# Kernel tuning notes

Measured on AMD Instinct MI355X. Metric: run time of the kernel, lower is better.

## Reference

```python
import jax, jax.numpy as jnp
import numpy as np

PATCH_SIZE = 3
CHANNELS = 1
SIGMA_RAW = 0.5
SIGMA_EFF = SIGMA_RAW * PATCH_SIZE ** 2  # sigma * patch_size**2 as in __init__


def setup_inputs() -> dict:
    key = jax.random.key(0)
    kx, ky = jax.random.split(key)
    N, C, H, W = 64, CHANNELS, 64, 64
    x = jax.random.normal(kx, (N, C, H, W), dtype=jnp.float32)
    y = jax.random.normal(ky, (N, C, H, W), dtype=jnp.float32)
    return {"x": x, "y": y}


def _pairwise_patch_distance(A, B):
    # A: (N_A, C, H, W), B: (N_B, C, H, W)
    N_A, C, H, W = A.shape
    N_B = B.shape[0]
    # broadcast pairwise squared pixel diffs: (N_A, N_B, C, H, W)
    pixel_diff = (A[:, None] - B[None]) ** 2
    kern = jnp.ones((1, C, PATCH_SIZE, PATCH_SIZE), dtype=A.dtype)  # OIHW
    d = jax.lax.conv_general_dilated(
        pixel_diff.reshape(N_A * N_B, C, H, W), kern,
        window_strides=(1, 1), padding='VALID',
        dimension_numbers=('NCHW', 'OIHW', 'NCHW'))
    H_new, W_new = d.shape[-2], d.shape[-1]
    return d.reshape(N_A, N_B, H_new, W_new)


def _gaussian_kernel(D):
    return jnp.exp(-D / (2.0 * SIGMA_EFF ** 2))


def _off_mean(K):
    # K: (N, N, h, w); mean over all off-diagonal (i != j) entries
    N, _, h, w = K.shape
    mask = ~jnp.eye(N, dtype=bool)
    total = jnp.sum(jnp.where(mask[:, :, None, None], K, jnp.zeros((), K.dtype)))
    count = (N * (N - 1)) * h * w
    return total / count


def reference(x, y):
    K_xx = _gaussian_kernel(_pairwise_patch_distance(x, x))
    K_xy = _gaussian_kernel(_pairwise_patch_distance(x, y))
    K_yy = _gaussian_kernel(_pairwise_patch_distance(y, y))
    return _off_mean(K_xx) - 2.0 * jnp.mean(K_xy) + _off_mean(K_yy)
```

## Files before the change

kernel.cpp:

```cpp
#include <hip/hip_runtime.h>


typedef __attribute__((ext_vector_type(8))) short short8v;
typedef __attribute__((ext_vector_type(4))) float f32x4;

#define NPOS 3844
#define WSTR 26
#define NBLK 992

#if __has_builtin(__builtin_amdgcn_exp2f)
#define EXP2F(v) __builtin_amdgcn_exp2f(v)
#else
#define EXP2F(v) __expf((v) * 0.69314718055994530942f)
#endif

template<int CTRL>
__device__ __forceinline__ float dpp0_f(float v) {
    int r = __builtin_amdgcn_update_dpp(0, __float_as_int(v), CTRL, 0xf, 0xf, true);
    return __int_as_float(r);
}
template<int CTRL, int RM>
__device__ __forceinline__ float dppm_f(float v) {
    int r = __builtin_amdgcn_update_dpp(0, __float_as_int(v), CTRL, RM, 0xf, true);
    return __int_as_float(r);
}
__device__ __forceinline__ float wave_reduce_f(float v) {
    v += dpp0_f<0x111>(v);
    v += dpp0_f<0x112>(v);
    v += dpp0_f<0x114>(v);
    v += dpp0_f<0x118>(v);
    v += dppm_f<0x142, 0xa>(v);
    v += dppm_f<0x143, 0xc>(v);
    return v;
}
__device__ __forceinline__ unsigned int bf16rne(float f) {
    unsigned int u = __float_as_uint(f);
    return (u + 0x7fffu + ((u >> 16) & 1u)) >> 16;
}

__global__ __launch_bounds__(256, 4) void mmd_fused_kernel(
    const float* __restrict__ x, const float* __restrict__ y,
    float* __restrict__ part)
{
    const int t = threadIdx.x, wid = t >> 6, lane = t & 63;
    const int p  = blockIdx.x >> 4;
    const int qg = blockIdx.x & 15;
    const int q  = qg * 4 + wid;

    __shared__ unsigned short win[128 * WSTR];
    __shared__ unsigned short rec[4 * 128 * 8];
    __shared__ unsigned short rec8[4 * 128];
    __shared__ float pren[4 * 128];
    __shared__ float wred[3][4];

    const float NS   = -1.0f / (40.5f * 0.69314718055994530942f);
    const float M2NS = -2.0f * NS;

    {
        const int cg1 = (qg < 15) ? qg + 1 : 15;
        #pragma unroll
        for (int k = 0; k < 3; ++k) {
            int it = t + k * 256;
            int n = it / 6, rem = it % 6;
            int u = rem >> 1, cg = rem & 1;
            const float* img = (n < 64) ? (x + n * 4096) : (y + (n - 64) * 4096);
            float4 v = *reinterpret_cast<const float4*>(
                img + (p + u) * 64 + ((cg ? cg1 : qg) << 2));
            unsigned int d0 = bf16rne(v.x) | (bf16rne(v.y) << 16);
            unsigned int d1 = bf16rne(v.z) | (bf16rne(v.w) << 16);
            unsigned int* w32 = reinterpret_cast<unsigned int*>(
                &win[n * WSTR + u * 8 + cg * 4]);
            w32[0] = d0; w32[1] = d1;
        }
    }
    __syncthreads();

    #pragma unroll
    for (int k = 0; k < 2; ++k) {
        int rid = t + k * 256;
        int ql = rid >> 7, n = rid & 127;
        const unsigned short* wp = &win[n * WSTR + ql];
        unsigned short b[9];
        #pragma unroll
        for (int u = 0; u < 3; ++u) {
            b[u * 3 + 0] = wp[u * 8 + 0];
            b[u * 3 + 1] = wp[u * 8 + 1];
            b[u * 3 + 2] = wp[u * 8 + 2];
        }
        float pre = 0.f;
        #pragma unroll
        for (int e = 0; e < 9; ++e) {
            float fv = __uint_as_float((unsigned)b[e] << 16);
            pre = fmaf(fv, fv, pre);
        }
        uint4 pk;
        pk.x = b[0] | ((unsigned)b[1] << 16);
        pk.y = b[2] | ((unsigned)b[3] << 16);
        pk.z = b[4] | ((unsigned)b[5] << 16);
        pk.w = b[6] | ((unsigned)b[7] << 16);
        *reinterpret_cast<uint4*>(&rec[(size_t)rid * 8]) = pk;
        rec8[rid] = b[8];
        pren[rid] = pre * NS;
    }
    __syncthreads();

    const int r = lane & 15, kg = lane >> 4;
    short8v frag[8];
    #pragma unroll
    for (int g = 0; g < 8; ++g) {
        short8v f = {0, 0, 0, 0, 0, 0, 0, 0};
        if (kg == 0)
            f = *reinterpret_cast<const short8v*>(&rec[(size_t)(wid * 128 + g * 16 + r) * 8]);
        else if (kg == 1)
            f[0] = (short)rec8[wid * 128 + g * 16 + r];
        frag[g] = f;
    }
    float pa[8][4], pb[8];
    #pragma unroll
    for (int g = 0; g < 8; ++g) {
        const float* pp = &pren[wid * 128 + g * 16 + kg * 4];
        pa[g][0] = pp[0]; pa[g][1] = pp[1]; pa[g][2] = pp[2]; pa[g][3] = pp[3];
        pb[g] = pren[wid * 128 + g * 16 + r];
    }

    const f32x4 zf = {0.f, 0.f, 0.f, 0.f};
    float ad0 = 0.f, ad1 = 0.f, as0 = 0.f, as1 = 0.f, ac0 = 0.f, ac1 = 0.f;

    #pragma unroll
    for (int g = 0; g < 8; ++g) {
        f32x4 c4 = __builtin_amdgcn_mfma_f32_16x16x32_bf16(frag[g], frag[g], zf, 0, 0, 0);
        float e = 0.f;
        #pragma unroll
        for (int m = 0; m < 4; ++m)
            e += EXP2F(fmaf(c4[m], M2NS, pa[g][m] + pb[g]));
        if (g & 1) ad1 += e; else ad0 += e;
    }

    #pragma unroll
    for (int ti = 1; ti < 8; ++ti)
        #pragma unroll
        for (int tj = 0; tj < ti; ++tj) {
            f32x4 c4 = __builtin_amdgcn_mfma_f32_16x16x32_bf16(frag[ti], frag[tj], zf, 0, 0, 0);
            float e = 0.f;
            #pragma unroll
            for (int m = 0; m < 4; ++m)
                e += EXP2F(fmaf(c4[m], M2NS, pa[ti][m] + pb[tj]));
            if (ti >= 4 && tj < 4) { if (tj & 1) ac1 += e; else ac0 += e; }
            else                   { if (tj & 1) as1 += e; else as0 += e; }
        }

    float acc_diag  = wave_reduce_f(ad0 + ad1);
    float acc_same  = wave_reduce_f(as0 + as1);
    float acc_cross = wave_reduce_f(ac0 + ac1);
    if (lane == 63) {
        const bool valid = (q < 62);
        wred[0][wid] = valid ? acc_diag  : 0.f;
        wred[1][wid] = valid ? acc_same  : 0.f;
        wred[2][wid] = valid ? acc_cross : 0.f;
    }
    __syncthreads();
    if (t == 0) {
        #pragma unroll
        for (int c = 0; c < 3; ++c)
            part[c * NBLK + blockIdx.x] =
                (wred[c][0] + wred[c][1]) + (wred[c][2] + wred[c][3]);
    }
}

__global__ __launch_bounds__(256) void mmd_final_kernel(
    const float* __restrict__ part, float* __restrict__ out)
{
    const int t = threadIdx.x;
    double sd = 0.0, ss = 0.0, sc = 0.0;
    #pragma unroll
    for (int k = 0; k < 4; ++k) {
        int e = t + k * 256;
        if (e < NBLK) {
            sd += (double)part[e];
            ss += (double)part[NBLK + e];
            sc += (double)part[2 * NBLK + e];
        }
    }
    #pragma unroll
    for (int off = 32; off > 0; off >>= 1) {
        sd += __shfl_xor(sd, off);
        ss += __shfl_xor(ss, off);
        sc += __shfl_xor(sc, off);
    }
    __shared__ double w[3][4];
    const int lane = t & 63, wd = t >> 6;
    if (lane == 0) { w[0][wd] = sd; w[1][wd] = ss; w[2][wd] = sc; }
    __syncthreads();
    if (t == 0) {
        double Sd = w[0][0] + w[0][1] + w[0][2] + w[0][3];
        double Ss = w[1][0] + w[1][1] + w[1][2] + w[1][3];
        double Sc = w[2][0] + w[2][1] + w[2][2] + w[2][3];
        double S_off = (Sd - 128.0 * (double)NPOS) + 2.0 * Ss;
        const double cnt_off = 64.0 * 63.0 * 62.0 * 62.0;
        const double cnt_all = 64.0 * 64.0 * 62.0 * 62.0;
        out[0] = (float)(S_off / cnt_off - 2.0 * Sc / cnt_all);
    }
}

extern "C" void kernel_launch(void* const* d_in, const int* in_sizes, int n_in,
                              void* d_out, int out_size, void* d_ws, size_t ws_size,
                              hipStream_t stream) {
    const float* x = (const float*)d_in[0];
    const float* y = (const float*)d_in[1];
    float* out  = (float*)d_out;
    float* part = (float*)d_ws;

    mmd_fused_kernel<<<62 * 16, 256, 0, stream>>>(x, y, part);
    mmd_final_kernel<<<1, 256, 0, stream>>>(part, out);
}
```

Measured before the change: 18.01 us.

## Switch to f16 MFMA and fold final reduction into main kernel via atomics

Replaces the bf16 16x16x32 MFMA with the f16 16x16x16 MFMA, padding each 9-element patch to 16 halves so each lane loads a 4-half fragment without branching. It also removes the second reduction kernel: each block atomically adds its three partial sums into global doubles, and the last block (found via an atomic counter) computes the output. This drops one kernel launch but adds a memset, atomics and a fence, and f16 changes the precision and range of the inputs.

```diff
diff --git a/kernel.cpp b/kernel.cpp
--- a/kernel.cpp
+++ b/kernel.cpp
@@ -1,7 +1,8 @@
 #include <hip/hip_runtime.h>
+#include <hip/hip_fp16.h>
 
 
-typedef __attribute__((ext_vector_type(8))) short short8v;
+typedef __attribute__((ext_vector_type(4))) _Float16 half4v;
 typedef __attribute__((ext_vector_type(4))) float f32x4;
 
 #define NPOS 3844
@@ -33,14 +34,19 @@
     v += dppm_f<0x143, 0xc>(v);
     return v;
 }
-__device__ __forceinline__ unsigned int bf16rne(float f) {
-    unsigned int u = __float_as_uint(f);
-    return (u + 0x7fffu + ((u >> 16) & 1u)) >> 16;
+__device__ __forceinline__ unsigned short f16bits(float f) {
+    __half h = __float2half(f);
+    return *reinterpret_cast<unsigned short*>(&h);
+}
+__device__ __forceinline__ float f16tof(unsigned short u) {
+    __half h = *reinterpret_cast<__half*>(&u);
+    return __half2float(h);
 }
 
 __global__ __launch_bounds__(256, 4) void mmd_fused_kernel(
     const float* __restrict__ x, const float* __restrict__ y,
-    float* __restrict__ part)
+    double* __restrict__ gacc, unsigned int* __restrict__ gcnt,
+    float* __restrict__ out)
 {
     const int t = threadIdx.x, wid = t >> 6, lane = t & 63;
     const int p  = blockIdx.x >> 4;
@@ -48,8 +54,7 @@
     const int q  = qg * 4 + wid;
 
     __shared__ unsigned short win[128 * WSTR];
-    __shared__ unsigned short rec[4 * 128 * 8];
-    __shared__ unsigned short rec8[4 * 128];
+    __shared__ unsigned short rec[4 * 128 * 16];
     __shared__ float pren[4 * 128];
     __shared__ float wred[3][4];
 
@@ -66,8 +71,8 @@
             const float* img = (n < 64) ? (x + n * 4096) : (y + (n - 64) * 4096);
             float4 v = *reinterpret_cast<const float4*>(
                 img + (p + u) * 64 + ((cg ? cg1 : qg) << 2));
-            unsigned int d0 = bf16rne(v.x) | (bf16rne(v.y) << 16);
-            unsigned int d1 = bf16rne(v.z) | (bf16rne(v.w) << 16);
+            unsigned int d0 = f16bits(v.x) | ((unsigned)f16bits(v.y) << 16);
+            unsigned int d1 = f16bits(v.z) | ((unsigned)f16bits(v.w) << 16);
             unsigned int* w32 = reinterpret_cast<unsigned int*>(
                 &win[n * WSTR + u * 8 + cg * 4]);
             w32[0] = d0; w32[1] = d1;
@@ -90,7 +95,7 @@
         float pre = 0.f;
         #pragma unroll
         for (int e = 0; e < 9; ++e) {
-            float fv = __uint_as_float((unsigned)b[e] << 16);
+            float fv = f16tof(b[e]);
             pre = fmaf(fv, fv, pre);
         }
         uint4 pk;
@@ -98,23 +103,21 @@
         pk.y = b[2] | ((unsigned)b[3] << 16);
         pk.z = b[4] | ((unsigned)b[5] << 16);
         pk.w = b[6] | ((unsigned)b[7] << 16);
-        *reinterpret_cast<uint4*>(&rec[(size_t)rid * 8]) = pk;
-        rec8[rid] = b[8];
+        uint4 pk2;
+        pk2.x = (unsigned)b[8]; pk2.y = 0u; pk2.z = 0u; pk2.w = 0u;
+        uint4* dst = reinterpret_cast<uint4*>(&rec[(size_t)rid * 16]);
+        dst[0] = pk; dst[1] = pk2;
         pren[rid] = pre * NS;
     }
     __syncthreads();
 
     const int r = lane & 15, kg = lane >> 4;
-    short8v frag[8];
+    half4v frag[8];
     #pragma unroll
-    for (int g = 0; g < 8; ++g) {
-        short8v f = {0, 0, 0, 0, 0, 0, 0, 0};
-        if (kg == 0)
-            f = *reinterpret_cast<const short8v*>(&rec[(size_t)(wid * 128 + g * 16 + r) * 8]);
-        else if (kg == 1)
-            f[0] = (short)rec8[wid * 128 + g * 16 + r];
-        frag[g] = f;
-    }
+    for (int g = 0; g < 8; ++g)
+        frag[g] = *reinterpret_cast<const half4v*>(
+            &rec[(size_t)(wid * 128 + g * 16 + r) * 16 + kg * 4]);
+
     float pa[8][4], pb[8];
     #pragma unroll
     for (int g = 0; g < 8; ++g) {
@@ -128,7 +131,7 @@
 
     #pragma unroll
     for (int g = 0; g < 8; ++g) {
-        f32x4 c4 = __builtin_amdgcn_mfma_f32_16x16x32_bf16(frag[g], frag[g], zf, 0, 0, 0);
+        f32x4 c4 = __builtin_amdgcn_mfma_f32_16x16x16f16(frag[g], frag[g], zf, 0, 0, 0);
         float e = 0.f;
         #pragma unroll
         for (int m = 0; m < 4; ++m)
@@ -140,7 +143,7 @@
     for (int ti = 1; ti < 8; ++ti)
         #pragma unroll
         for (int tj = 0; tj < ti; ++tj) {
-            f32x4 c4 = __builtin_amdgcn_mfma_f32_16x16x32_bf16(frag[ti], frag[tj], zf, 0, 0, 0);
+            f32x4 c4 = __builtin_amdgcn_mfma_f32_16x16x16f16(frag[ti], frag[tj], zf, 0, 0, 0);
             float e = 0.f;
             #pragma unroll
             for (int m = 0; m < 4; ++m)
@@ -159,46 +162,25 @@
         wred[2][wid] = valid ? acc_cross : 0.f;
     }
     __syncthreads();
+
     if (t == 0) {
-        #pragma unroll
-        for (int c = 0; c < 3; ++c)
-            part[c * NBLK + blockIdx.x] =
-                (wred[c][0] + wred[c][1]) + (wred[c][2] + wred[c][3]);
-    }
-}
-
-__global__ __launch_bounds__(256) void mmd_final_kernel(
-    const float* __restrict__ part, float* __restrict__ out)
-{
-    const int t = threadIdx.x;
-    double sd = 0.0, ss = 0.0, sc = 0.0;
-    #pragma unroll
-    for (int k = 0; k < 4; ++k) {
-        int e = t + k * 256;
-        if (e < NBLK) {
-            sd += (double)part[e];
-            ss += (double)part[NBLK + e];
-            sc += (double)part[2 * NBLK + e];
+        double sd = (double)((wred[0][0] + wred[0][1]) + (wred[0][2] + wred[0][3]));
+        double ss = (double)((wred[1][0] + wred[1][1]) + (wred[1][2] + wred[1][3]));
+        double sc = (double)((wred[2][0] + wred[2][1]) + (wred[2][2] + wred[2][3]));
+        atomicAdd(&gacc[0], sd);
+        atomicAdd(&gacc[1], ss);
+        atomicAdd(&gacc[2], sc);
+        __threadfence();
+        unsigned int tick = atomicAdd(gcnt, 1u);
+        if (tick == NBLK - 1) {
+            double Sd = atomicAdd(&gacc[0], 0.0);
+            double Ss = atomicAdd(&gacc[1], 0.0);
+            double Sc = atomicAdd(&gacc[2], 0.0);
+            double S_off = (Sd - 128.0 * (double)NPOS) + 2.0 * Ss;
+            const double cnt_off = 64.0 * 63.0 * 62.0 * 62.0;
+            const double cnt_all = 64.0 * 64.0 * 62.0 * 62.0;
+            out[0] = (float)(S_off / cnt_off - 2.0 * Sc / cnt_all);
         }
-    }
-    #pragma unroll
-    for (int off = 32; off > 0; off >>= 1) {
-        sd += __shfl_xor(sd, off);
-        ss += __shfl_xor(ss, off);
-        sc += __shfl_xor(sc, off);
-    }
-    __shared__ double w[3][4];
-    const int lane = t & 63, wd = t >> 6;
-    if (lane == 0) { w[0][wd] = sd; w[1][wd] = ss; w[2][wd] = sc; }
-    __syncthreads();
-    if (t == 0) {
-        double Sd = w[0][0] + w[0][1] + w[0][2] + w[0][3];
-        double Ss = w[1][0] + w[1][1] + w[1][2] + w[1][3];
-        double Sc = w[2][0] + w[2][1] + w[2][2] + w[2][3];
-        double S_off = (Sd - 128.0 * (double)NPOS) + 2.0 * Ss;
-        const double cnt_off = 64.0 * 63.0 * 62.0 * 62.0;
-        const double cnt_all = 64.0 * 64.0 * 62.0 * 62.0;
-        out[0] = (float)(S_off / cnt_off - 2.0 * Sc / cnt_all);
     }
 }
 
@@ -207,9 +189,10 @@
                               hipStream_t stream) {
     const float* x = (const float*)d_in[0];
     const float* y = (const float*)d_in[1];
-    float* out  = (float*)d_out;
-    float* part = (float*)d_ws;
+    float* out = (float*)d_out;
+    double* gacc = (double*)d_ws;
+    unsigned int* gcnt = (unsigned int*)(gacc + 3);
 
-    mmd_fused_kernel<<<62 * 16, 256, 0, stream>>>(x, y, part);
-    mmd_final_kernel<<<1, 256, 0, stream>>>(part, out);
+    (void)hipMemsetAsync(d_ws, 0, 32, stream);
+    mmd_fused_kernel<<<NBLK, 256, 0, stream>>>(x, y, gacc, gcnt, out);
 }
```

Measured after the change: 64.11 us. 3.56x slower.
